# Kernel tuning notes

Measured on AMD Instinct MI355X. Metric: run time of the kernel, lower is better.

The kernel has to match this reference:

```python
import jax, jax.numpy as jnp
import numpy as np

H, U = 64, 64  # matrix-completion patch size; system size is (H*U)^2 = 4096^2


def svtC(X, tau):
    # Singular value thresholding: soft-threshold singular values by tau.
    u, s, vt = jnp.linalg.svd(X, full_matrices=False)
    return (u * jax.nn.relu(s - tau)) @ vt


def setup_inputs() -> dict:
    key = jax.random.key(0)
    ks = jax.random.split(key, 12)
    x = jax.random.normal(ks[0], (H, U), jnp.float32)
    L = jax.random.normal(ks[1], (H, U), jnp.float32)
    entries_mask = jax.random.randint(ks[2], (H, U), 0, 2).astype(bool)
    # D_tilda: symmetric PSD (HU, HU) smoothness operator so the system is well-conditioned
    M = jax.random.normal(ks[3], (H * U, H * U), jnp.float32)
    D_tilda = (M @ M.T) / jnp.float32(H * U)
    th_P = jax.random.normal(ks[4], (H, U), jnp.float32)
    v = jax.random.normal(ks[5], (), jnp.float32)
    coef_gamma = jax.random.uniform(ks[6], (), jnp.float32)
    neta = jax.random.uniform(ks[7], (), jnp.float32)
    lamda1 = jax.random.uniform(ks[8], (), jnp.float32)
    lamda2 = jax.random.uniform(ks[9], (), jnp.float32)
    rho = jax.random.uniform(ks[10], (), jnp.float32) + jnp.float32(0.1)
    S = jax.random.normal(ks[11], (H, H), jnp.float32) / np.float32(np.sqrt(H))
    return {"x": x, "L": L, "entries_mask": entries_mask, "D_tilda": D_tilda,
            "th_P": th_P, "v": v, "coef_gamma": coef_gamma, "neta": neta,
            "lamda1": lamda1, "lamda2": lamda2, "rho": rho, "S": S}


def reference(x, L, entries_mask, D_tilda, th_P, v, coef_gamma, neta,
              lamda1, lamda2, rho, S):
    tau = jax.nn.sigmoid(v) * coef_gamma
    # Q_tilda = diag(vec(mask)); S_tilda = kron(I_U, S^T S)
    q = entries_mask.astype(jnp.float32).reshape(-1)  # (HU,)
    StS = S.T @ S                                      # (H, H)
    S_tilda = jnp.kron(jnp.eye(U, dtype=jnp.float32), StS)  # (HU, HU)
    eye = jnp.eye(H * U, dtype=jnp.float32)
    A = jnp.diag(q) + lamda1 * D_tilda + lamda2 * S_tilda + rho * eye
    vec = rho * (L - th_P) + jnp.where(entries_mask, x, jnp.float32(0.0))
    # Original uses explicit dense inverse followed by matvec
    Xtmp = (jnp.linalg.inv(A) @ vec.reshape(-1)).reshape(H, U)
    Ltmp = svtC(Xtmp + th_P, tau)
    Ptmp = th_P + neta * (Xtmp - Ltmp)
    return Ltmp, Ptmp
```

## Files before the change

### kernel.cpp

```cpp
#include <hip/hip_runtime.h>
#include <cstddef>

#define HU    4096
#define NBLK  256
#define NTHR  512
#define MAXIT 100
#define TOL2  1e-7f
#define NARR  32

#define WS_STS  0
#define WS_DINV 4096
#define WS_R0   8192
#define WS_U0   12288
#define WS_W    16384
#define WS_DEL  24576
#define WS_BAR  (WS_DEL + (MAXIT + 2) * 64)
#define WS_FLAG (WS_BAR + NARR * 16)
#define WS_END  (WS_FLAG + 8 * 16)

typedef _Float16 half4v __attribute__((ext_vector_type(4)));

__device__ __forceinline__ float fastrcp(float x) {
  float r; asm("v_rcp_f32 %0, %1" : "=v"(r) : "v"(x)); return r;
}
__device__ __forceinline__ float fastsqrt(float x) {
  float r; asm("v_sqrt_f32 %0, %1" : "=v"(r) : "v"(x)); return r;
}
__device__ __forceinline__ float fastrsq(float x) {
  float r; asm("v_rsq_f32 %0, %1" : "=v"(r) : "v"(x)); return r;
}

__device__ __forceinline__ float waveReduce(float v) {
#pragma unroll
  for (int off = 32; off > 0; off >>= 1) v += __shfl_xor(v, off, 64);
  return v;
}
__device__ __forceinline__ unsigned waveReduceU(unsigned v) {
#pragma unroll
  for (int off = 32; off > 0; off >>= 1) v += __shfl_xor((int)v, off, 64);
  return v;
}

__device__ __forceinline__ float blockSum(float v, float* red) {
  v = waveReduce(v);
  if ((threadIdx.x & 63) == 0) red[threadIdx.x >> 6] = v;
  __syncthreads();
  float s = 0.f;
#pragma unroll
  for (int i = 0; i < 8; ++i) s += red[i];
  __syncthreads();
  return s;
}

__device__ __forceinline__ void gsync(unsigned* cnt, unsigned* flg, unsigned gen) {
  __syncthreads();
  const int b = blockIdx.x;
  if (b == 0) {
    if (threadIdx.x < 64) {
      if (threadIdx.x == 0) {
        __threadfence();
        __hip_atomic_fetch_add(&cnt[0], 1u, __ATOMIC_RELEASE, __HIP_MEMORY_SCOPE_AGENT);
      }
      const unsigned target = gen * NBLK;
      for (;;) {
        unsigned s = (threadIdx.x < NARR)
          ? __hip_atomic_load(&cnt[threadIdx.x * 16], __ATOMIC_RELAXED, __HIP_MEMORY_SCOPE_AGENT)
          : 0u;
        if (waveReduceU(s) >= target) break;
        __builtin_amdgcn_s_sleep(1);
      }
      __threadfence();
      if (threadIdx.x < 8)
        __hip_atomic_store(&flg[threadIdx.x * 16], gen,
                           __ATOMIC_RELEASE, __HIP_MEMORY_SCOPE_AGENT);
    }
  } else if (threadIdx.x == 0) {
    __threadfence();
    __hip_atomic_fetch_add(&cnt[(b & (NARR - 1)) * 16], 1u,
                           __ATOMIC_RELEASE, __HIP_MEMORY_SCOPE_AGENT);
    const int fl = (b & 7) * 16;
    while (__hip_atomic_load(&flg[fl], __ATOMIC_RELAXED, __HIP_MEMORY_SCOPE_AGENT) < gen)
      __builtin_amdgcn_s_sleep(1);
    __threadfence();
  }
  __syncthreads();
}

#define SWP 6
#define S_W 68

__device__ __forceinline__ float red16(float x) {
  int t;
  t = __builtin_amdgcn_update_dpp(0, __float_as_int(x), 0x128, 0xF, 0xF, false);
  x += __int_as_float(t);
  t = __builtin_amdgcn_update_dpp(0, __float_as_int(x), 0x124, 0xF, 0xF, false);
  x += __int_as_float(t);
  t = __builtin_amdgcn_update_dpp(0, __float_as_int(x), 0x122, 0xF, 0xF, false);
  x += __int_as_float(t);
  t = __builtin_amdgcn_update_dpp(0, __float_as_int(x), 0x121, 0xF, 0xF, false);
  x += __int_as_float(t);
  return x;
}

__device__ __forceinline__ int gf8mul(int a, int b) {
  int p = 0;
  if (b & 1) p ^= a;
  if (b & 2) p ^= (a << 1);
  if (b & 4) p ^= (a << 2);
  if (p & 16) p ^= 22;
  if (p & 8)  p ^= 11;
  return p;
}

__device__ __forceinline__ int sel8(const int c[8], int i) {
  int r = c[0];
  r = (i == 1) ? c[1] : r;
  r = (i == 2) ? c[2] : r;
  r = (i == 3) ? c[3] : r;
  r = (i == 4) ? c[4] : r;
  r = (i == 5) ? c[5] : r;
  r = (i == 6) ? c[6] : r;
  r = (i == 7) ? c[7] : r;
  return r;
}

__global__ void __launch_bounds__(NTHR, 1)
fused_kernel(const float* __restrict__ x_in, const float* __restrict__ L_in,
             const int* __restrict__ mask, const float* __restrict__ D,
             const float* __restrict__ thP, const float* __restrict__ S,
             const float* __restrict__ l1p, const float* __restrict__ l2p,
             const float* __restrict__ rhop, const float* __restrict__ vp,
             const float* __restrict__ cgp, const float* __restrict__ netap,
             float* __restrict__ ws, float* __restrict__ out)
{
  __shared__ __align__(16) float u_l[HU];
  __shared__ __align__(16) char pool[128 * 1024];
  __shared__ float red[8];
  __shared__ float g_s[64];
  unsigned* cnt  = (unsigned*)(ws + WS_BAR);
  unsigned* flg  = (unsigned*)(ws + WS_FLAG);
  const float* sts = ws + WS_STS;
  const float lam1 = *l1p, lam2 = *l2p, rho = *rhop;
  const int tid = threadIdx.x, b = blockIdx.x;
  const int wv = tid >> 6, lane = tid & 63;
  unsigned gen = 0;

  const int gtid = b * NTHR + tid;
  if (gtid < HU) {
    const int a = gtid >> 6, c = gtid & 63;
    float acc = 0.f, sdiag = 0.f;
    for (int h = 0; h < 64; ++h) {
      const float sa = S[h * 64 + a], sc = S[h * 64 + c];
      acc = fmaf(sa, sc, acc);
      sdiag = fmaf(sc, sc, sdiag);
    }
    ws[WS_STS + gtid] = acc;
    const float q = mask[gtid] ? 1.f : 0.f;
    const float diag = q + rho + lam1 * D[(size_t)gtid * (HU + 1)] + lam2 * sdiag;
    const float bb = rho * (L_in[gtid] - thP[gtid]) + (mask[gtid] ? x_in[gtid] : 0.f);
    const float di = 1.f / diag;
    ws[WS_DINV + gtid] = di;
    ws[WS_R0 + gtid] = bb;
    ws[WS_U0 + gtid] = bb * di;
  }

  {
    const float4* __restrict__ Dg = (const float4*)(D + (size_t)b * 16 * HU);
    half4v* __restrict__ Dh4 = (half4v*)pool;
    for (int o = tid; o < 16 * HU / 4; o += NTHR) {
      const float4 dv = Dg[o];
      half4v h;
      h[0] = (_Float16)dv.x; h[1] = (_Float16)dv.y;
      h[2] = (_Float16)dv.z; h[3] = (_Float16)dv.w;
      Dh4[o] = h;
    }
  }
  gsync(cnt, flg, ++gen);

  float r_reg[8], s_reg[8], dinv_reg[8];
  float acc0 = 0.f;
#pragma unroll
  for (int m = 0; m < 8; ++m) {
    const int i = tid + m * NTHR;
    const float rv = ws[WS_R0 + i], uv = ws[WS_U0 + i];
    r_reg[m] = rv; u_l[i] = uv; dinv_reg[m] = ws[WS_DINV + i];
    s_reg[m] = 0.f;
  }
  __syncthreads();
#pragma unroll
  for (int m = 0; m < 8; ++m) acc0 = fmaf(r_reg[m], u_l[tid + m * NTHR], acc0);
  const float gamma0 = blockSum(acc0, red);

  float p_arr[8], x_arr[8];
#pragma unroll
  for (int m = 0; m < 8; ++m) { p_arr[m] = 0.f; x_arr[m] = 0.f; }

  const int row0 = b * 16 + wv * 2;
  const int iq = row0 >> 6, j0 = row0 & 63;
  const float4* __restrict__ u4 = (const float4*)u_l;
  const float m0 = mask[row0] ? 1.f : 0.f;
  const float m1 = mask[row0 + 1] ? 1.f : 0.f;
  const float sts0 = sts[j0 * 64 + lane];
  const float sts1 = sts[j0 * 64 + 64 + lane];
  const float dex0 = D[(size_t)row0 * (HU + 1)];
  const float dex1 = D[(size_t)(row0 + 1) * (HU + 1)];
  const float diagf0 = m0 + rho + lam1 * (dex0 - (float)(_Float16)dex0);
  const float diagf1 = m1 + rho + lam1 * (dex1 - (float)(_Float16)dex1);
  const half4v* __restrict__ H0 = (const half4v*)((_Float16*)pool + (size_t)(wv * 2) * HU);
  const half4v* __restrict__ H1 = H0 + (HU / 4);

  float gamma = gamma0, gamma_prev = 1.f, alpha_prev = 1.f;
  for (int k = 0; k < MAXIT; ++k) {
    float* __restrict__ wbuf = ws + WS_W + (k & 1) * HU;
    {
      float acc_a = 0.f, acc_b = 0.f;
#pragma unroll
      for (int it = 0; it < 16; ++it) {
        const float4 uu = u4[it * 64 + lane];
        const half4v d0 = H0[it * 64 + lane];
        const half4v d1 = H1[it * 64 + lane];
        acc_a = fmaf((float)d0[0], uu.x, acc_a); acc_a = fmaf((float)d0[1], uu.y, acc_a);
        acc_a = fmaf((float)d0[2], uu.z, acc_a); acc_a = fmaf((float)d0[3], uu.w, acc_a);
        acc_b = fmaf((float)d1[0], uu.x, acc_b); acc_b = fmaf((float)d1[1], uu.y, acc_b);
        acc_b = fmaf((float)d1[2], uu.z, acc_b); acc_b = fmaf((float)d1[3], uu.w, acc_b);
      }
      const float us = u_l[iq * 64 + lane];
      float t0 = fmaf(lam1, acc_a, lam2 * (sts0 * us));
      float t1 = fmaf(lam1, acc_b, lam2 * (sts1 * us));
      t0 = waveReduce(t0);
      t1 = waveReduce(t1);
      const float u0v = u_l[row0], u1v = u_l[row0 + 1];
      const float w0 = t0 + diagf0 * u0v;
      const float w1 = t1 + diagf1 * u1v;
      if (lane == 0) {
        wbuf[row0] = w0;
        wbuf[row0 + 1] = w1;
        red[wv] = fmaf(w0, u0v, w1 * u1v);
      }
      __syncthreads();
      if (tid == 0) {
        float s = 0.f;
#pragma unroll
        for (int k2 = 0; k2 < 8; ++k2) s += red[k2];
        atomicAdd(&ws[WS_DEL + k * 64 + (b & 63)], s);
      }
    }
    gsync(cnt, flg, ++gen);

    if (wv == 0) {
      const float dv = __hip_atomic_load(&ws[WS_DEL + k * 64 + lane],
                                         __ATOMIC_RELAXED, __HIP_MEMORY_SCOPE_AGENT);
      const float w = waveReduce(dv);
      if (lane == 0) red[0] = w;
    }
    __syncthreads();
    const float dk = red[0];
    __syncthreads();

    const float beta  = (k == 0) ? 0.f : gamma * fastrcp(gamma_prev);
    const float denom = (k == 0) ? dk  : (dk - beta * gamma * fastrcp(alpha_prev));
    const float alpha = gamma * fastrcp(denom);

    float acc = 0.f;
#pragma unroll
    for (int m = 0; m < 8; ++m) {
      const int i = tid + m * NTHR;
      const float uold = u_l[i];
      const float wvv = wbuf[i];
      const float sv = (k == 0) ? wvv : fmaf(beta, s_reg[m], wvv);
      s_reg[m] = sv;
      const float rv = fmaf(-alpha, sv, r_reg[m]);
      r_reg[m] = rv;
      const float uv = rv * dinv_reg[m];
      u_l[i] = uv;
      acc = fmaf(rv, uv, acc);
      const float pk = (k == 0) ? uold : fmaf(beta, p_arr[m], uold);
      p_arr[m] = pk;
      x_arr[m] = fmaf(alpha, pk, x_arr[m]);
    }
    const float gnext = blockSum(acc, red);

    gamma_prev = gamma;
    alpha_prev = alpha;
    gamma = gnext;
    if (!(gnext > TOL2 * gamma0)) break;
  }

  if (b != 0) return;

  float* Wl = (float*)pool;
  float* Yr = Wl + 64 * S_W;
  float* T1 = Yr + 64 * S_W;
  float* Wr = T1 + 64 * S_W;
  __syncthreads();

  float t0acc = 0.f;
#pragma unroll
  for (int mm = 0; mm < 8; ++mm) {
    const int i = tid + mm * NTHR;
    const int rr = i >> 6, cc = i & 63;
    const float y = x_arr[mm] + thP[i];
    Wl[cc * S_W + rr] = y;
    Yr[rr * S_W + cc] = y;
    t0acc = fmaf(y, y, t0acc);
  }
  const float T0 = blockSum(t0acc, red);
  const float thr = 1.6e-10f * T0 * T0;

  const int team = lane >> 4;
  const int sub  = lane & 15;

  for (int sweep = 0; sweep < SWP; ++sweep) {
    float offacc = 0.f;
    for (int mr = 0; mr < 9; ++mr) {
      int cols[8];
#pragma unroll
      for (int j = 0; j < 8; ++j)
        cols[j] = (mr == 8) ? (8 * wv + j) : (8 * j + (gf8mul(mr, j) ^ wv));
      for (int r = 0; r < 7; ++r) {
        const int pi = (team == 0) ? 7 : ((r + team) % 7);
        const int qi = (team == 0) ? (r % 7) : ((r + 7 - team) % 7);
        const int cp = sel8(cols, pi);
        const int cq = sel8(cols, qi);
        float4* wp = (float4*)(Wl + cp * S_W) + sub;
        float4* wq = (float4*)(Wl + cq * S_W) + sub;
        const float4 a = *wp, bb = *wq;
        float dpp = fmaf(a.x, a.x, fmaf(a.y, a.y, fmaf(a.z, a.z, a.w * a.w)));
        float dqq = fmaf(bb.x, bb.x, fmaf(bb.y, bb.y, fmaf(bb.z, bb.z, bb.w * bb.w)));
        float dpq = fmaf(a.x, bb.x, fmaf(a.y, bb.y, fmaf(a.z, bb.z, a.w * bb.w)));
        dpp = red16(dpp); dqq = red16(dqq); dpq = red16(dpq);
        offacc = fmaf(dpq, dpq, offacc);
        if (dpq * dpq > 1e-14f * dpp * dqq) {
          const float th = (dqq - dpp) * 0.5f * fastrcp(dpq);
          const float sg = (th >= 0.f) ? 1.f : -1.f;
          const float t  = sg * fastrcp(fabsf(th) + fastsqrt(fmaf(th, th, 1.f)));
          const float c1 = fastrsq(fmaf(t, t, 1.f));
          const float s1 = t * c1;
          float4 na, nb;
          na.x = c1 * a.x - s1 * bb.x;  nb.x = s1 * a.x + c1 * bb.x;
          na.y = c1 * a.y - s1 * bb.y;  nb.y = s1 * a.y + c1 * bb.y;
          na.z = c1 * a.z - s1 * bb.z;  nb.z = s1 * a.z + c1 * bb.z;
          na.w = c1 * a.w - s1 * bb.w;  nb.w = s1 * a.w + c1 * bb.w;
          *wp = na; *wq = nb;
        }
      }
      __syncthreads();
    }
    const float tot = blockSum(offacc, red);
    if (sweep >= 2 && tot < thr) break;
  }

  if (tid < 64) {
    const float4* wc = (const float4*)(Wl + tid * S_W);
    float nn = 0.f;
#pragma unroll
    for (int i2 = 0; i2 < 16; ++i2) {
      const float4 u = wc[i2];
      nn = fmaf(u.x, u.x, fmaf(u.y, u.y, fmaf(u.z, u.z, fmaf(u.w, u.w, nn))));
    }
    const float sv = sqrtf(nn);
    const float tau = (*cgp) / (1.f + expf(-(*vp)));
    g_s[tid] = (sv > tau) ? (sv - tau) / (sv * nn) : 0.f;
  }
  __syncthreads();

  const int j = tid & 63;
  const int ib = tid >> 6;

#pragma unroll
  for (int mm = 0; mm < 8; ++mm) {
    const int k = ib + 8 * mm;
    const float4* wcol = (const float4*)(Wl + k * S_W);
    float acc = 0.f;
#pragma unroll
    for (int i4 = 0; i4 < 16; ++i4) {
      const float4 wvv = wcol[i4];
      acc = fmaf(wvv.x, Yr[(4 * i4 + 0) * S_W + j], acc);
      acc = fmaf(wvv.y, Yr[(4 * i4 + 1) * S_W + j], acc);
      acc = fmaf(wvv.z, Yr[(4 * i4 + 2) * S_W + j], acc);
      acc = fmaf(wvv.w, Yr[(4 * i4 + 3) * S_W + j], acc);
    }
    T1[k * S_W + j] = acc;
  }
  for (int o = tid; o < 4096; o += 512) {
    const int i2 = o >> 6, kk = o & 63;
    Wr[i2 * S_W + kk] = Wl[kk * S_W + i2] * g_s[kk];
  }
  __syncthreads();

  const float neta = *netap;
#pragma unroll
  for (int mm = 0; mm < 8; ++mm) {
    const int i2 = ib + 8 * mm;
    const float4* wrow = (const float4*)(Wr + i2 * S_W);
    float acc = 0.f;
#pragma unroll
    for (int k4 = 0; k4 < 16; ++k4) {
      const float4 wvv = wrow[k4];
      acc = fmaf(wvv.x, T1[(4 * k4 + 0) * S_W + j], acc);
      acc = fmaf(wvv.y, T1[(4 * k4 + 1) * S_W + j], acc);
      acc = fmaf(wvv.z, T1[(4 * k4 + 2) * S_W + j], acc);
      acc = fmaf(wvv.w, T1[(4 * k4 + 3) * S_W + j], acc);
    }
    const int o = i2 * 64 + j;
    out[o] = acc;
    out[4096 + o] = thP[o] + neta * (x_arr[mm] - acc);
  }
}

extern "C" void kernel_launch(void* const* d_in, const int* in_sizes, int n_in,
                              void* d_out, int out_size, void* d_ws, size_t ws_size,
                              hipStream_t stream)
{
  const float* x_in  = (const float*)d_in[0];
  const float* L_in  = (const float*)d_in[1];
  const int*   mask  = (const int*)d_in[2];
  const float* D     = (const float*)d_in[3];
  const float* thP   = (const float*)d_in[4];
  const float* vp    = (const float*)d_in[5];
  const float* cgp   = (const float*)d_in[6];
  const float* netap = (const float*)d_in[7];
  const float* l1p   = (const float*)d_in[8];
  const float* l2p   = (const float*)d_in[9];
  const float* rhop  = (const float*)d_in[10];
  const float* S     = (const float*)d_in[11];
  float* ws  = (float*)d_ws;
  float* out = (float*)d_out;

  hipMemsetAsync(ws + WS_DEL, 0, (WS_END - WS_DEL) * sizeof(float), stream);

  void* args[] = { (void*)&x_in, (void*)&L_in, (void*)&mask, (void*)&D, (void*)&thP,
                   (void*)&S, (void*)&l1p, (void*)&l2p, (void*)&rhop,
                   (void*)&vp, (void*)&cgp, (void*)&netap, (void*)&ws, (void*)&out };
  hipLaunchCooperativeKernel((void*)fused_kernel, dim3(NBLK), dim3(NTHR),
                             args, 0, stream);
}
```

Baseline: 332.6 us.

## Fuse grid barrier with dot-product reduction via per-block generation-tagged slots

Replaces the counter/flag grid barrier and separate atomicAdd reduction with a single all-to-all exchange: each block writes a 64-bit slot holding a generation tag and its partial dot product. Every block then polls all 256 slots and sums them locally. This removes the master-block relay and the atomic reduction, cutting barrier latency per CG iteration. It also skips the p/x accumulation on blocks other than 0, since only block 0 uses them. The cost is more polling traffic from every block reading all slots.

Result: slower. 346.3 us (+4.1%).

```diff
diff --git a/kernel.cpp b/kernel.cpp
--- a/kernel.cpp
+++ b/kernel.cpp
@@ -6,17 +6,14 @@
 #define NTHR  512
 #define MAXIT 100
 #define TOL2  1e-7f
-#define NARR  32
 
 #define WS_STS  0
 #define WS_DINV 4096
 #define WS_R0   8192
 #define WS_U0   12288
 #define WS_W    16384
-#define WS_DEL  24576
-#define WS_BAR  (WS_DEL + (MAXIT + 2) * 64)
-#define WS_FLAG (WS_BAR + NARR * 16)
-#define WS_END  (WS_FLAG + 8 * 16)
+#define WS_BAR  24576
+#define WS_END  (WS_BAR + 2 * 256 * 2)
 
 typedef _Float16 half4v __attribute__((ext_vector_type(4)));
 
@@ -33,11 +30,6 @@
 __device__ __forceinline__ float waveReduce(float v) {
 #pragma unroll
   for (int off = 32; off > 0; off >>= 1) v += __shfl_xor(v, off, 64);
-  return v;
-}
-__device__ __forceinline__ unsigned waveReduceU(unsigned v) {
-#pragma unroll
-  for (int off = 32; off > 0; off >>= 1) v += __shfl_xor((int)v, off, 64);
   return v;
 }
 
@@ -52,38 +44,48 @@
   return s;
 }
 
-__device__ __forceinline__ void gsync(unsigned* cnt, unsigned* flg, unsigned gen) {
-  __syncthreads();
-  const int b = blockIdx.x;
-  if (b == 0) {
-    if (threadIdx.x < 64) {
-      if (threadIdx.x == 0) {
-        __threadfence();
-        __hip_atomic_fetch_add(&cnt[0], 1u, __ATOMIC_RELEASE, __HIP_MEMORY_SCOPE_AGENT);
+__device__ __forceinline__ float gsync_dk(unsigned long long* slots, unsigned gen,
+                                          float* red) {
+  __syncthreads();
+  const int tid = threadIdx.x, lane = tid & 63;
+  unsigned long long* arr = slots + (gen & 1) * 256;
+  if (tid < 64) {
+    if (lane == 0) {
+      float s = 0.f;
+#pragma unroll
+      for (int i = 0; i < 8; ++i) s += red[i];
+      __threadfence();
+      __hip_atomic_store(&arr[blockIdx.x],
+                         ((unsigned long long)gen << 32) | __float_as_uint(s),
+                         __ATOMIC_RELEASE, __HIP_MEMORY_SCOPE_AGENT);
+    }
+    float dsum;
+    for (;;) {
+      const unsigned long long v0 = __hip_atomic_load(&arr[lane],
+                                      __ATOMIC_RELAXED, __HIP_MEMORY_SCOPE_AGENT);
+      const unsigned long long v1 = __hip_atomic_load(&arr[lane + 64],
+                                      __ATOMIC_RELAXED, __HIP_MEMORY_SCOPE_AGENT);
+      const unsigned long long v2 = __hip_atomic_load(&arr[lane + 128],
+                                      __ATOMIC_RELAXED, __HIP_MEMORY_SCOPE_AGENT);
+      const unsigned long long v3 = __hip_atomic_load(&arr[lane + 192],
+                                      __ATOMIC_RELAXED, __HIP_MEMORY_SCOPE_AGENT);
+      const bool ok = ((unsigned)(v0 >> 32) >= gen) && ((unsigned)(v1 >> 32) >= gen)
+                   && ((unsigned)(v2 >> 32) >= gen) && ((unsigned)(v3 >> 32) >= gen);
+      if (__all(ok)) {
+        dsum = __uint_as_float((unsigned)v0) + __uint_as_float((unsigned)v1)
+             + __uint_as_float((unsigned)v2) + __uint_as_float((unsigned)v3);
+        break;
       }
-      const unsigned target = gen * NBLK;
-      for (;;) {
-        unsigned s = (threadIdx.x < NARR)
-          ? __hip_atomic_load(&cnt[threadIdx.x * 16], __ATOMIC_RELAXED, __HIP_MEMORY_SCOPE_AGENT)
-          : 0u;
-        if (waveReduceU(s) >= target) break;
-        __builtin_amdgcn_s_sleep(1);
-      }
-      __threadfence();
-      if (threadIdx.x < 8)
-        __hip_atomic_store(&flg[threadIdx.x * 16], gen,
-                           __ATOMIC_RELEASE, __HIP_MEMORY_SCOPE_AGENT);
-    }
-  } else if (threadIdx.x == 0) {
+      __builtin_amdgcn_s_sleep(1);
+    }
+    const float dk = waveReduce(dsum);
     __threadfence();
-    __hip_atomic_fetch_add(&cnt[(b & (NARR - 1)) * 16], 1u,
-                           __ATOMIC_RELEASE, __HIP_MEMORY_SCOPE_AGENT);
-    const int fl = (b & 7) * 16;
-    while (__hip_atomic_load(&flg[fl], __ATOMIC_RELAXED, __HIP_MEMORY_SCOPE_AGENT) < gen)
-      __builtin_amdgcn_s_sleep(1);
-    __threadfence();
-  }
-  __syncthreads();
+    if (lane == 0) red[0] = dk;
+  }
+  __syncthreads();
+  const float dk = red[0];
+  __syncthreads();
+  return dk;
 }
 
 #define SWP 6
@@ -137,8 +139,7 @@
   __shared__ __align__(16) char pool[128 * 1024];
   __shared__ float red[8];
   __shared__ float g_s[64];
-  unsigned* cnt  = (unsigned*)(ws + WS_BAR);
-  unsigned* flg  = (unsigned*)(ws + WS_FLAG);
+  unsigned long long* slots = (unsigned long long*)(ws + WS_BAR);
   const float* sts = ws + WS_STS;
   const float lam1 = *l1p, lam2 = *l2p, rho = *rhop;
   const int tid = threadIdx.x, b = blockIdx.x;
@@ -175,7 +176,8 @@
       Dh4[o] = h;
     }
   }
-  gsync(cnt, flg, ++gen);
+  if (tid < 8) red[tid] = 0.f;
+  gsync_dk(slots, ++gen, red);
 
   float r_reg[8], s_reg[8], dinv_reg[8];
   float acc0 = 0.f;
@@ -237,25 +239,8 @@
         wbuf[row0 + 1] = w1;
         red[wv] = fmaf(w0, u0v, w1 * u1v);
       }
-      __syncthreads();
-      if (tid == 0) {
-        float s = 0.f;
-#pragma unroll
-        for (int k2 = 0; k2 < 8; ++k2) s += red[k2];
-        atomicAdd(&ws[WS_DEL + k * 64 + (b & 63)], s);
-      }
-    }
-    gsync(cnt, flg, ++gen);
-
-    if (wv == 0) {
-      const float dv = __hip_atomic_load(&ws[WS_DEL + k * 64 + lane],
-                                         __ATOMIC_RELAXED, __HIP_MEMORY_SCOPE_AGENT);
-      const float w = waveReduce(dv);
-      if (lane == 0) red[0] = w;
-    }
-    __syncthreads();
-    const float dk = red[0];
-    __syncthreads();
+    }
+    const float dk = gsync_dk(slots, ++gen, red);
 
     const float beta  = (k == 0) ? 0.f : gamma * fastrcp(gamma_prev);
     const float denom = (k == 0) ? dk  : (dk - beta * gamma * fastrcp(alpha_prev));
@@ -274,9 +259,11 @@
       const float uv = rv * dinv_reg[m];
       u_l[i] = uv;
       acc = fmaf(rv, uv, acc);
-      const float pk = (k == 0) ? uold : fmaf(beta, p_arr[m], uold);
-      p_arr[m] = pk;
-      x_arr[m] = fmaf(alpha, pk, x_arr[m]);
+      if (b == 0) {
+        const float pk = (k == 0) ? uold : fmaf(beta, p_arr[m], uold);
+        p_arr[m] = pk;
+        x_arr[m] = fmaf(alpha, pk, x_arr[m]);
+      }
     }
     const float gnext = blockSum(acc, red);
 
@@ -427,7 +414,7 @@
   float* ws  = (float*)d_ws;
   float* out = (float*)d_out;
 
-  hipMemsetAsync(ws + WS_DEL, 0, (WS_END - WS_DEL) * sizeof(float), stream);
+  hipMemsetAsync(ws + WS_BAR, 0, (WS_END - WS_BAR) * sizeof(float), stream);
 
   void* args[] = { (void*)&x_in, (void*)&L_in, (void*)&mask, (void*)&D, (void*)&thP,
                    (void*)&S, (void*)&l1p, (void*)&l2p, (void*)&rhop,
```
